# Optimization experiments

Measured on AMD Instinct MI355X. Metric: run time of the kernel, lower is better.

Reference implementation:

```python
import jax, jax.numpy as jnp
import numpy as np

B, N, D, H, O = 8, 2048, 64, 64, 64
ALPHA = 2.0  # LeakyReLU negative slope per module default
NEG = -9e15


def _lin(x, W, b):
    # torch nn.Linear: y = x @ W.T + b, W is [out, in]
    return x @ W.T + b


def setup_inputs() -> dict:
    key = jax.random.key(0)
    ks = jax.random.split(key, 32)
    f32 = jnp.float32
    x = jax.random.normal(ks[0], (B, N, D), f32)
    adj = jax.random.randint(ks[1], (B, N, N), 0, 2).astype(f32)
    c = jax.random.normal(ks[2], (B, N, H), f32)
    h = jax.random.normal(ks[3], (B, N, H), f32)
    s = 0.1
    W = jax.random.normal(ks[4], (D, H), f32) * s           # GAT weight
    a = jax.random.normal(ks[5], (2 * H, 1), f32) * s       # GAT attention vector
    def lin(k, out_d, in_d):
        k1, k2 = jax.random.split(k)
        return (jax.random.normal(k1, (out_d, in_d), f32) * s,
                jax.random.normal(k2, (out_d,), f32) * s)
    Wf, bWf = lin(ks[6], H, H); Wi, bWi = lin(ks[7], H, H)
    Wo, bWo = lin(ks[8], H, H); Wc, bWc = lin(ks[9], H, H)
    Uf, bUf = lin(ks[10], H, D); Ui, bUi = lin(ks[11], H, D)
    Uo, bUo = lin(ks[12], H, D); Uc, bUc = lin(ks[13], H, D)
    Wout, bout = lin(ks[14], O, 2 * H)
    return dict(x=x, adj=adj, c=c, h=h, W=W, a=a,
                Wf=Wf, bWf=bWf, Wi=Wi, bWi=bWi, Wo=Wo, bWo=bWo, Wc=Wc, bWc=bWc,
                Uf=Uf, bUf=bUf, Ui=Ui, bUi=bUi, Uo=Uo, bUo=bUo, Uc=Uc, bUc=bUc,
                Wout=Wout, bout=bout)


def reference(x, adj, c, h, W, a,
              Wf, bWf, Wi, bWi, Wo, bWo, Wc, bWc,
              Uf, bUf, Ui, bUi, Uo, bUo, Uc, bUc,
              Wout, bout):
    # ---- GraphAttentionLayer (eval mode: dropout is identity) ----
    Wh = x @ W                                   # [B,N,H]
    # e[b,i,j] = leakyrelu(a[:H].Wh_i + a[H:].Wh_j) -- same math as the
    a_src = (Wh @ a[:H]).squeeze(-1)             # [B,N]
    a_dst = (Wh @ a[H:]).squeeze(-1)             # [B,N]
    e = jax.nn.leaky_relu(a_src[:, :, None] + a_dst[:, None, :], ALPHA)  # [B,N,N]
    att = jnp.where(adj > 0, e, NEG)
    att = jax.nn.softmax(att, axis=2)
    x_hidden = jax.nn.elu(att @ Wh)              # [B,N,H] (concat=True)
    # ---- LSTMLayer step ----
    f_t = jax.nn.sigmoid(_lin(h, Wf, bWf) + _lin(x, Uf, bUf))
    i_t = jax.nn.sigmoid(_lin(h, Wi, bWi) + _lin(x, Ui, bUi))
    o_t = jax.nn.sigmoid(_lin(h, Wo, bWo) + _lin(x, Uo, bUo))
    c_hat = jnp.tanh(_lin(h, Wc, bWc) + _lin(x, Uc, bUc))
    c_t = f_t * c + i_t * c_hat
    h_t = o_t * jax.nn.relu(c_t)                 # gate = nn.ReLU() default
    total = jnp.concatenate([x_hidden, h_t], axis=2)  # [B,N,2H]
    output = jax.nn.relu(_lin(total, Wout, bout))     # [B,N,O]
    return (output, h_t, c_t)
```

## Files before the change

### kernel.cpp

```cpp
#include <hip/hip_runtime.h>
#include <math.h>

#define B_ 8
#define N_ 2048
#define NT_ (B_*N_)
#define OUTSZ (NT_*64)

#define WS_ASRC  0
#define WS_ADST  (WS_ASRC + NT_)
#define WS_WT    (WS_ADST + NT_)
#define WS_BB    (WS_WT + 128*256)
#define WS_WOT   (WS_BB + 256)
#define WS_PD    (WS_WOT + 128*64)
#define WS_PN    (WS_PD + 8*NT_)

typedef float f32x4 __attribute__((ext_vector_type(4)));
typedef __bf16 bf16x8 __attribute__((ext_vector_type(8)));
typedef __bf16 bf16x4 __attribute__((ext_vector_type(4)));

__device__ __forceinline__ float lrelu2(float x) { return x > 0.f ? x : 2.f * x; }
__device__ __forceinline__ float f4get(const float4& v, int k) { return k==0?v.x:(k==1?v.y:(k==2?v.z:v.w)); }

__global__ __launch_bounds__(256) void k1_wh(const float* __restrict__ x, const float* __restrict__ W,
                                             const float* __restrict__ a, float* __restrict__ ws,
                                             __bf16* __restrict__ whT,
                                             const float* Wf, const float* Wi, const float* Wo, const float* Wc,
                                             const float* Uf, const float* Ui, const float* Uo, const float* Uc,
                                             const float* bWf, const float* bWi, const float* bWo, const float* bWc,
                                             const float* bUf, const float* bUi, const float* bUo, const float* bUc,
                                             const float* Wout)
{
    __shared__ float xl[64 * 68];
    __shared__ float Wl[64 * 68];
    int t = threadIdx.x;
    if (blockIdx.x >= 256) {
        int idx = (blockIdx.x - 256) * 256 + t;
        if (idx < 128 * 256) {
            int k = idx >> 8, o = idx & 255;
            int g = o >> 6, u = o & 63;
            const float* Wg = (g == 0) ? Wf : (g == 1) ? Wi : (g == 2) ? Wo : Wc;
            const float* Ug = (g == 0) ? Uf : (g == 1) ? Ui : (g == 2) ? Uo : Uc;
            ws[WS_WT + idx] = (k < 64) ? Wg[u * 64 + k] : Ug[u * 64 + (k - 64)];
        } else if (idx < 128 * 256 + 256) {
            int o = idx - 128 * 256;
            int g = o >> 6, u = o & 63;
            const float* bW = (g == 0) ? bWf : (g == 1) ? bWi : (g == 2) ? bWo : bWc;
            const float* bU = (g == 0) ? bUf : (g == 1) ? bUi : (g == 2) ? bUo : bUc;
            ws[WS_BB + o] = bW[u] + bU[u];
        } else if (idx < 128 * 256 + 256 + 128 * 64) {
            int j = idx - (128 * 256 + 256);
            int k = j >> 6, u = j & 63;
            ws[WS_WOT + j] = Wout[u * 128 + k];
        }
        return;
    }
    int i0 = blockIdx.x * 64;
    #pragma unroll
    for (int it = 0; it < 4; ++it) {
        int f = t + 256 * it;
        int r = f >> 4, q = f & 15;
        *(float4*)&xl[r * 68 + q * 4] = *(const float4*)&x[i0 * 64 + f * 4];
        *(float4*)&Wl[r * 68 + q * 4] = *(const float4*)&W[f * 4];
    }
    __syncthreads();
    int cg = t & 15, rg = t >> 4;
    int c0 = cg * 4, r0 = rg * 4;
    float acc[4][4] = {};
    #pragma unroll
    for (int d0 = 0; d0 < 64; d0 += 4) {
        float4 wv[4], xv[4];
        #pragma unroll
        for (int k = 0; k < 4; ++k) wv[k] = *(float4*)&Wl[(d0 + k) * 68 + c0];
        #pragma unroll
        for (int ri = 0; ri < 4; ++ri) xv[ri] = *(float4*)&xl[(r0 + ri) * 68 + d0];
        #pragma unroll
        for (int ri = 0; ri < 4; ++ri)
            #pragma unroll
            for (int k = 0; k < 4; ++k) {
                float xs = f4get(xv[ri], k);
                acc[ri][0] += xs * wv[k].x; acc[ri][1] += xs * wv[k].y;
                acc[ri][2] += xs * wv[k].z; acc[ri][3] += xs * wv[k].w;
            }
    }
    int b = i0 >> 11;
    int rowb0 = (i0 & 2047) + r0;
    #pragma unroll
    for (int cj = 0; cj < 4; ++cj) {
        bf16x4 v;
        v[0] = (__bf16)acc[0][cj]; v[1] = (__bf16)acc[1][cj];
        v[2] = (__bf16)acc[2][cj]; v[3] = (__bf16)acc[3][cj];
        *(bf16x4*)&whT[((size_t)(b * 64 + c0 + cj)) * N_ + rowb0] = v;
    }
    float4 a0 = *(const float4*)&a[c0];
    float4 a1 = *(const float4*)&a[64 + c0];
    #pragma unroll
    for (int ri = 0; ri < 4; ++ri) {
        int row = i0 + r0 + ri;
        float s0 = acc[ri][0]*a0.x + acc[ri][1]*a0.y + acc[ri][2]*a0.z + acc[ri][3]*a0.w;
        float s1 = acc[ri][0]*a1.x + acc[ri][1]*a1.y + acc[ri][2]*a1.z + acc[ri][3]*a1.w;
        #pragma unroll
        for (int m = 1; m < 16; m <<= 1) { s0 += __shfl_xor(s0, m, 64); s1 += __shfl_xor(s1, m, 64); }
        if (cg == 0) { ws[WS_ASRC + row] = s0; ws[WS_ADST + row] = s1; }
    }
}

__global__ __launch_bounds__(256) void k2v10(const float* __restrict__ adj,
                                             const __bf16* __restrict__ whT,
                                             float* __restrict__ ws)
{
    __shared__ __bf16 adjt[2][16][268];
    __shared__ float lsa[4][16][68];
    __shared__ float lsd[4][16];
    __shared__ float gred[4];
    int tid = threadIdx.x;
    int lane = tid & 63, w = tid >> 6;
    int r = lane & 15, g = lane >> 4;
    int jr = blockIdx.x & 7;
    int rslab = blockIdx.x >> 3;
    int b = rslab >> 4;
    int row_base = rslab * 128;
    int jbeg = jr * 256 + w * 64;

    {
        float gm = -3.0e38f;
        for (int i = tid; i < N_; i += 256) gm = fmaxf(gm, ws[WS_ADST + b * N_ + i]);
        #pragma unroll
        for (int m_ = 1; m_ < 64; m_ <<= 1) gm = fmaxf(gm, __shfl_xor(gm, m_, 64));
        if (lane == 0) gred[w] = gm;
    }
    __syncthreads();
    float gmax = fmaxf(fmaxf(gred[0], gred[1]), fmaxf(gred[2], gred[3]));

    bf16x8 bfr[2][4];
    #pragma unroll
    for (int ks = 0; ks < 2; ++ks)
        #pragma unroll
        for (int n = 0; n < 4; ++n)
            bfr[ks][n] = *(const bf16x8*)&whT[(size_t)(b * 64 + n * 16 + r) * N_ + jbeg + ks * 32 + g * 8];
    float ejr[2][8];
    #pragma unroll
    for (int ks = 0; ks < 2; ++ks) {
        float4 d0 = *(const float4*)&ws[WS_ADST + b * N_ + jbeg + ks * 32 + g * 8];
        float4 d1 = *(const float4*)&ws[WS_ADST + b * N_ + jbeg + ks * 32 + g * 8 + 4];
        ejr[ks][0]=__expf(d0.x); ejr[ks][1]=__expf(d0.y); ejr[ks][2]=__expf(d0.z); ejr[ks][3]=__expf(d0.w);
        ejr[ks][4]=__expf(d1.x); ejr[ks][5]=__expf(d1.y); ejr[ks][6]=__expf(d1.z); ejr[ks][7]=__expf(d1.w);
    }
    float asv8[8];
    #pragma unroll
    for (int tt = 0; tt < 8; ++tt)
        asv8[tt] = ws[WS_ASRC + row_base + tt * 16 + r];

    f32x4 sreg[2][4];

#define SLOAD(T, S)                                                                        \
    {                                                                                      \
        _Pragma("unroll")                                                                  \
        for (int i = 0; i < 4; ++i)                                                        \
            sreg[S][i] = *(const f32x4*)&adj[(size_t)(row_base + (T) * 16 + w * 4 + i) * N_ \
                                             + jr * 256 + lane * 4];                       \
    }
#define SWRITE(T, S)                                                                       \
    {                                                                                      \
        _Pragma("unroll")                                                                  \
        for (int i = 0; i < 4; ++i) {                                                      \
            bf16x4 bv;                                                                     \
            bv[0] = (__bf16)sreg[S][i][0]; bv[1] = (__bf16)sreg[S][i][1];                  \
            bv[2] = (__bf16)sreg[S][i][2]; bv[3] = (__bf16)sreg[S][i][3];                  \
            *(bf16x4*)&adjt[(T) & 1][w * 4 + i][lane * 4] = bv;                            \
        }                                                                                  \
    }

    SLOAD(0, 0);
    SWRITE(0, 0);
    SLOAD(1, 1);
    asm volatile("s_waitcnt lgkmcnt(0)" ::: "memory");
    __builtin_amdgcn_s_barrier();
    asm volatile("" ::: "memory");

    __bf16* pn = (__bf16*)&ws[WS_PN];

    #pragma unroll
    for (int t = 0; t < 8; ++t) {
        const int s = t & 1;
        if (t + 2 < 8) { SLOAD(t + 2, s); }
        float as = asv8[t];
        float M  = lrelu2(as + gmax);
        float c1 = __expf(as - M);
        float c2 = __expf(2.f * as - M);
        float thr = __expf(-as);
        f32x4 acc[4] = {{0.f,0.f,0.f,0.f},{0.f,0.f,0.f,0.f},{0.f,0.f,0.f,0.f},{0.f,0.f,0.f,0.f}};
        float dsum = 0.f;
        #pragma unroll
        for (int ks = 0; ks < 2; ++ks) {
            bf16x8 at = *(const bf16x8*)&adjt[s][r][w * 64 + ks * 32 + g * 8];
            bf16x8 af;
            float ds_ = 0.f;
            #pragma unroll
            for (int e = 0; e < 8; ++e) {
                float avv = (float)at[e];
                float E = ejr[ks][e];
                float p = (E > thr) ? c1 * E : (c2 * E) * E;
                p = (avv > 0.f) ? p : 0.f;
                ds_ += p;
                af[e] = (__bf16)p;
            }
            dsum += ds_;
            #pragma unroll
            for (int n = 0; n < 4; ++n)
                acc[n] = __builtin_amdgcn_mfma_f32_16x16x32_bf16(af, bfr[ks][n], acc[n], 0, 0, 0);
        }
        dsum += __shfl_xor(dsum, 16, 64);
        dsum += __shfl_xor(dsum, 32, 64);
        #pragma unroll
        for (int n = 0; n < 4; ++n)
            #pragma unroll
            for (int i = 0; i < 4; ++i)
                lsa[w][g * 4 + i][n * 16 + r] = acc[n][i];
        if (g == 0) lsd[w][r] = dsum;
        if (t + 1 < 8) { SWRITE(t + 1, s ^ 1); }
        asm volatile("s_waitcnt lgkmcnt(0)" ::: "memory");
        __builtin_amdgcn_s_barrier();
        asm volatile("" ::: "memory");
        {
            int rl = tid >> 4, h0 = (tid & 15) * 4;
            float4 sv = make_float4(0.f, 0.f, 0.f, 0.f);
            #pragma unroll
            for (int w2 = 0; w2 < 4; ++w2) {
                float4 q = *(const float4*)&lsa[w2][rl][h0];
                sv.x += q.x; sv.y += q.y; sv.z += q.z; sv.w += q.w;
            }
            int row0 = row_base + t * 16;
            bf16x4 bv;
            bv[0] = (__bf16)sv.x; bv[1] = (__bf16)sv.y; bv[2] = (__bf16)sv.z; bv[3] = (__bf16)sv.w;
            *(bf16x4*)&pn[((size_t)jr * NT_ + row0 + rl) * 64 + h0] = bv;
            if (tid < 16)
                ws[WS_PD + jr * NT_ + row0 + tid] =
                    lsd[0][tid] + lsd[1][tid] + lsd[2][tid] + lsd[3][tid];
        }
        asm volatile("s_waitcnt lgkmcnt(0)" ::: "memory");
        __builtin_amdgcn_s_barrier();
        asm volatile("" ::: "memory");
    }
#undef SLOAD
#undef SWRITE
}

__global__ __launch_bounds__(256) void k3_lstm(const float* __restrict__ x, const float* __restrict__ c,
                                               const float* __restrict__ h, const float* __restrict__ ws,
                                               float* __restrict__ out)
{
    __shared__ float Al[16 * 132];
    __shared__ float gl[16 * 260];
    int t = threadIdx.x;
    int base = blockIdx.x * 16;
    {
        int r = t >> 4, k0 = (t & 15) * 8;
        const float* src = (k0 < 64) ? &h[(base + r) * 64 + k0] : &x[(base + r) * 64 + (k0 - 64)];
        *(float4*)&Al[r * 132 + k0]     = *(const float4*)&src[0];
        *(float4*)&Al[r * 132 + k0 + 4] = *(const float4*)&src[4];
    }
    __syncthreads();
    int og = t & 63, rg = t >> 6;
    int o0 = og * 4;
    const float* WT = &ws[WS_WT];
    float acc[4][4] = {};
    #pragma unroll
    for (int k0 = 0; k0 < 128; k0 += 4) {
        float4 wv[4], av[4];
        #pragma unroll
        for (int kk = 0; kk < 4; ++kk) wv[kk] = *(const float4*)&WT[(k0 + kk) * 256 + o0];
        #pragma unroll
        for (int rr = 0; rr < 4; ++rr) av[rr] = *(float4*)&Al[(rg + 4 * rr) * 132 + k0];
        #pragma unroll
        for (int rr = 0; rr < 4; ++rr)
            #pragma unroll
            for (int kk = 0; kk < 4; ++kk) {
                float as = f4get(av[rr], kk);
                acc[rr][0] += as * wv[kk].x; acc[rr][1] += as * wv[kk].y;
                acc[rr][2] += as * wv[kk].z; acc[rr][3] += as * wv[kk].w;
            }
    }
    float4 bbv = *(const float4*)&ws[WS_BB + o0];
    #pragma unroll
    for (int rr = 0; rr < 4; ++rr) {
        int r = rg + 4 * rr;
        *(float4*)&gl[r * 260 + o0] = make_float4(acc[rr][0] + bbv.x, acc[rr][1] + bbv.y,
                                                  acc[rr][2] + bbv.z, acc[rr][3] + bbv.w);
    }
    __syncthreads();
    int u = t & 63, rq = t >> 6;
    #pragma unroll
    for (int pp = 0; pp < 4; ++pp) {
        int r = rq + 4 * pp;
        float gf = gl[r * 260 + u];
        float gi = gl[r * 260 + 64 + u];
        float go = gl[r * 260 + 128 + u];
        float gc = gl[r * 260 + 192 + u];
        float fg = 1.f / (1.f + __expf(-gf));
        float ig = 1.f / (1.f + __expf(-gi));
        float oo = 1.f / (1.f + __expf(-go));
        float ch = tanhf(gc);
        float cv = c[(base + r) * 64 + u];
        float ct = fg * cv + ig * ch;
        float ht = oo * fmaxf(ct, 0.f);
        out[OUTSZ + (base + r) * 64 + u] = ht;
        out[2 * OUTSZ + (base + r) * 64 + u] = ct;
    }
}

__global__ __launch_bounds__(256) void k5b(const float* __restrict__ ws, const float* __restrict__ bout,
                                           float* __restrict__ out)
{
    __shared__ float Al[16 * 132];
    int t = threadIdx.x;
    int base = blockIdx.x * 16;
    const float* ht = &out[OUTSZ];
    const __bf16* pn = (const __bf16*)&ws[WS_PN];
    #pragma unroll
    for (int it = 0; it < 2; ++it) {
        int f = t + 256 * it;
        int r = f >> 5, q = f & 31;
        int k0 = q * 4;
        int row = base + r;
        float4 v;
        if (k0 < 64) {
            float4 s = make_float4(0.f, 0.f, 0.f, 0.f);
            float d = 0.f;
            #pragma unroll
            for (int jr = 0; jr < 8; ++jr) {
                bf16x4 p = *(const bf16x4*)&pn[((size_t)jr * NT_ + row) * 64 + k0];
                s.x += (float)p[0]; s.y += (float)p[1]; s.z += (float)p[2]; s.w += (float)p[3];
                d += ws[WS_PD + jr * NT_ + row];
            }
            float inv = 1.f / d;
            v.x = s.x * inv; v.x = v.x > 0.f ? v.x : expm1f(v.x);
            v.y = s.y * inv; v.y = v.y > 0.f ? v.y : expm1f(v.y);
            v.z = s.z * inv; v.z = v.z > 0.f ? v.z : expm1f(v.z);
            v.w = s.w * inv; v.w = v.w > 0.f ? v.w : expm1f(v.w);
        } else {
            v = *(const float4*)&ht[(size_t)row * 64 + (k0 - 64)];
        }
        *(float4*)&Al[r * 132 + k0] = v;
    }
    __syncthreads();
    int row = t >> 4, cg = t & 15;
    int o0 = cg * 4;
    const float* WT = &ws[WS_WOT];
    float4 acc = make_float4(0.f, 0.f, 0.f, 0.f);
    #pragma unroll 8
    for (int k = 0; k < 128; ++k) {
        float a = Al[row * 132 + k];
        float4 wv = *(const float4*)&WT[k * 64 + o0];
        acc.x += a * wv.x; acc.y += a * wv.y; acc.z += a * wv.z; acc.w += a * wv.w;
    }
    float4 bo = *(const float4*)&bout[o0];
    float4 o;
    o.x = fmaxf(acc.x + bo.x, 0.f);
    o.y = fmaxf(acc.y + bo.y, 0.f);
    o.z = fmaxf(acc.z + bo.z, 0.f);
    o.w = fmaxf(acc.w + bo.w, 0.f);
    *(float4*)&out[(size_t)(base + row) * 64 + o0] = o;
}

extern "C" void kernel_launch(void* const* d_in, const int* in_sizes, int n_in,
                              void* d_out, int out_size, void* d_ws, size_t ws_size,
                              hipStream_t stream)
{
    const float* x    = (const float*)d_in[0];
    const float* adj  = (const float*)d_in[1];
    const float* c    = (const float*)d_in[2];
    const float* h    = (const float*)d_in[3];
    const float* W    = (const float*)d_in[4];
    const float* a    = (const float*)d_in[5];
    const float* Wf   = (const float*)d_in[6];
    const float* bWf  = (const float*)d_in[7];
    const float* Wi   = (const float*)d_in[8];
    const float* bWi  = (const float*)d_in[9];
    const float* Wo   = (const float*)d_in[10];
    const float* bWo  = (const float*)d_in[11];
    const float* Wc   = (const float*)d_in[12];
    const float* bWc  = (const float*)d_in[13];
    const float* Uf   = (const float*)d_in[14];
    const float* bUf  = (const float*)d_in[15];
    const float* Ui   = (const float*)d_in[16];
    const float* bUi  = (const float*)d_in[17];
    const float* Uo   = (const float*)d_in[18];
    const float* bUo  = (const float*)d_in[19];
    const float* Uc   = (const float*)d_in[20];
    const float* bUc  = (const float*)d_in[21];
    const float* Wout = (const float*)d_in[22];
    const float* bout = (const float*)d_in[23];
    float* out = (float*)d_out;
    float* ws  = (float*)d_ws;
    __bf16* whT = (__bf16*)out;

    k1_wh<<<417, 256, 0, stream>>>(x, W, a, ws, whT,
                                   Wf, Wi, Wo, Wc, Uf, Ui, Uo, Uc,
                                   bWf, bWi, bWo, bWc, bUf, bUi, bUo, bUc, Wout);
    k3_lstm<<<NT_ / 16, 256, 0, stream>>>(x, c, h, ws, out);
    k2v10<<<1024, 256, 0, stream>>>(adj, whT, ws);
    k5b<<<NT_ / 16, 256, 0, stream>>>(ws, bout, out);
}
```

Before: 85.84 us.

## Fuse Wh projection and LSTM step into one launch, split weight prep

Weight transposition and bias packing move into a small standalone prep kernel. The GAT Wh projection blocks and the LSTM gate blocks now run as one 1280-block launch that branches on block index and shares one shared-memory buffer. The two independent stages can then overlap on the GPU, which removes the launch gap and tail between them. In exchange, the LSTM blocks reserve the larger shared allocation, which may lower occupancy, and the launch count stays the same.

Result: no change. 86.78 us (+1.1%).

```diff
diff --git a/kernel.cpp b/kernel.cpp
--- a/kernel.cpp
+++ b/kernel.cpp
@@ -21,86 +21,150 @@
 __device__ __forceinline__ float lrelu2(float x) { return x > 0.f ? x : 2.f * x; }
 __device__ __forceinline__ float f4get(const float4& v, int k) { return k==0?v.x:(k==1?v.y:(k==2?v.z:v.w)); }
 
-__global__ __launch_bounds__(256) void k1_wh(const float* __restrict__ x, const float* __restrict__ W,
-                                             const float* __restrict__ a, float* __restrict__ ws,
-                                             __bf16* __restrict__ whT,
-                                             const float* Wf, const float* Wi, const float* Wo, const float* Wc,
-                                             const float* Uf, const float* Ui, const float* Uo, const float* Uc,
-                                             const float* bWf, const float* bWi, const float* bWo, const float* bWc,
-                                             const float* bUf, const float* bUi, const float* bUo, const float* bUc,
-                                             const float* Wout)
+__global__ void k0_prep(const float* Wf, const float* Wi, const float* Wo, const float* Wc,
+                        const float* Uf, const float* Ui, const float* Uo, const float* Uc,
+                        const float* bWf, const float* bWi, const float* bWo, const float* bWc,
+                        const float* bUf, const float* bUi, const float* bUo, const float* bUc,
+                        const float* Wout, float* ws)
 {
-    __shared__ float xl[64 * 68];
-    __shared__ float Wl[64 * 68];
+    int idx = blockIdx.x * 256 + threadIdx.x;
+    if (idx < 128 * 256) {
+        int k = idx >> 8, o = idx & 255;
+        int g = o >> 6, u = o & 63;
+        const float* Wg = (g == 0) ? Wf : (g == 1) ? Wi : (g == 2) ? Wo : Wc;
+        const float* Ug = (g == 0) ? Uf : (g == 1) ? Ui : (g == 2) ? Uo : Uc;
+        ws[WS_WT + idx] = (k < 64) ? Wg[u * 64 + k] : Ug[u * 64 + (k - 64)];
+    } else if (idx < 128 * 256 + 256) {
+        int o = idx - 128 * 256;
+        int g = o >> 6, u = o & 63;
+        const float* bW = (g == 0) ? bWf : (g == 1) ? bWi : (g == 2) ? bWo : bWc;
+        const float* bU = (g == 0) ? bUf : (g == 1) ? bUi : (g == 2) ? bUo : bUc;
+        ws[WS_BB + o] = bW[u] + bU[u];
+    } else if (idx < 128 * 256 + 256 + 128 * 64) {
+        int j = idx - (128 * 256 + 256);
+        int k = j >> 6, u = j & 63;
+        ws[WS_WOT + j] = Wout[u * 128 + k];
+    }
+}
+
+__global__ __launch_bounds__(256) void k13(const float* __restrict__ x, const float* __restrict__ W,
+                                           const float* __restrict__ a, float* __restrict__ ws,
+                                           __bf16* __restrict__ whT,
+                                           const float* __restrict__ c, const float* __restrict__ h,
+                                           float* __restrict__ out)
+{
+    __shared__ float smem[2 * 64 * 68];
     int t = threadIdx.x;
-    if (blockIdx.x >= 256) {
-        int idx = (blockIdx.x - 256) * 256 + t;
-        if (idx < 128 * 256) {
-            int k = idx >> 8, o = idx & 255;
-            int g = o >> 6, u = o & 63;
-            const float* Wg = (g == 0) ? Wf : (g == 1) ? Wi : (g == 2) ? Wo : Wc;
-            const float* Ug = (g == 0) ? Uf : (g == 1) ? Ui : (g == 2) ? Uo : Uc;
-            ws[WS_WT + idx] = (k < 64) ? Wg[u * 64 + k] : Ug[u * 64 + (k - 64)];
-        } else if (idx < 128 * 256 + 256) {
-            int o = idx - 128 * 256;
-            int g = o >> 6, u = o & 63;
-            const float* bW = (g == 0) ? bWf : (g == 1) ? bWi : (g == 2) ? bWo : bWc;
-            const float* bU = (g == 0) ? bUf : (g == 1) ? bUi : (g == 2) ? bUo : bUc;
-            ws[WS_BB + o] = bW[u] + bU[u];
-        } else if (idx < 128 * 256 + 256 + 128 * 64) {
-            int j = idx - (128 * 256 + 256);
-            int k = j >> 6, u = j & 63;
-            ws[WS_WOT + j] = Wout[u * 128 + k];
+
+    if (blockIdx.x < 256) {
+        float* xl = smem;
+        float* Wl = smem + 64 * 68;
+        int i0 = blockIdx.x * 64;
+        #pragma unroll
+        for (int it = 0; it < 4; ++it) {
+            int f = t + 256 * it;
+            int r = f >> 4, q = f & 15;
+            *(float4*)&xl[r * 68 + q * 4] = *(const float4*)&x[i0 * 64 + f * 4];
+            *(float4*)&Wl[r * 68 + q * 4] = *(const float4*)&W[f * 4];
+        }
+        __syncthreads();
+        int cg = t & 15, rg = t >> 4;
+        int c0 = cg * 4, r0 = rg * 4;
+        float acc[4][4] = {};
+        #pragma unroll
+        for (int d0 = 0; d0 < 64; d0 += 4) {
+            float4 wv[4], xv[4];
+            #pragma unroll
+            for (int k = 0; k < 4; ++k) wv[k] = *(float4*)&Wl[(d0 + k) * 68 + c0];
+            #pragma unroll
+            for (int ri = 0; ri < 4; ++ri) xv[ri] = *(float4*)&xl[(r0 + ri) * 68 + d0];
+            #pragma unroll
+            for (int ri = 0; ri < 4; ++ri)
+                #pragma unroll
+                for (int k = 0; k < 4; ++k) {
+                    float xs = f4get(xv[ri], k);
+                    acc[ri][0] += xs * wv[k].x; acc[ri][1] += xs * wv[k].y;
+                    acc[ri][2] += xs * wv[k].z; acc[ri][3] += xs * wv[k].w;
+                }
+        }
+        int b = i0 >> 11;
+        int rowb0 = (i0 & 2047) + r0;
+        #pragma unroll
+        for (int cj = 0; cj < 4; ++cj) {
+            bf16x4 v;
+            v[0] = (__bf16)acc[0][cj]; v[1] = (__bf16)acc[1][cj];
+            v[2] = (__bf16)acc[2][cj]; v[3] = (__bf16)acc[3][cj];
+            *(bf16x4*)&whT[((size_t)(b * 64 + c0 + cj)) * N_ + rowb0] = v;
+        }
+        float4 a0 = *(const float4*)&a[c0];
+        float4 a1 = *(const float4*)&a[64 + c0];
+        #pragma unroll
+        for (int ri = 0; ri < 4; ++ri) {
+            int row = i0 + r0 + ri;
+            float s0 = acc[ri][0]*a0.x + acc[ri][1]*a0.y + acc[ri][2]*a0.z + acc[ri][3]*a0.w;
+            float s1 = acc[ri][0]*a1.x + acc[ri][1]*a1.y + acc[ri][2]*a1.z + acc[ri][3]*a1.w;
+            #pragma unroll
+            for (int m = 1; m < 16; m <<= 1) { s0 += __shfl_xor(s0, m, 64); s1 += __shfl_xor(s1, m, 64); }
+            if (cg == 0) { ws[WS_ASRC + row] = s0; ws[WS_ADST + row] = s1; }
         }
         return;
     }
-    int i0 = blockIdx.x * 64;
-    #pragma unroll
-    for (int it = 0; it < 4; ++it) {
-        int f = t + 256 * it;
-        int r = f >> 4, q = f & 15;
-        *(float4*)&xl[r * 68 + q * 4] = *(const float4*)&x[i0 * 64 + f * 4];
-        *(float4*)&Wl[r * 68 + q * 4] = *(const float4*)&W[f * 4];
+
+    float* Al = smem;
+    float* gl = smem + 16 * 132;
+    int base = (blockIdx.x - 256) * 16;
+    {
+        int r = t >> 4, k0 = (t & 15) * 8;
+        const float* src = (k0 < 64) ? &h[(base + r) * 64 + k0] : &x[(base + r) * 64 + (k0 - 64)];
+        *(float4*)&Al[r * 132 + k0]     = *(const float4*)&src[0];
+        *(float4*)&Al[r * 132 + k0 + 4] = *(const float4*)&src[4];
     }
     __syncthreads();
-    int cg = t & 15, rg = t >> 4;
-    int c0 = cg * 4, r0 = rg * 4;
+    int og = t & 63, rg = t >> 6;
+    int o0 = og * 4;
+    const float* WT = &ws[WS_WT];
     float acc[4][4] = {};
     #pragma unroll
-    for (int d0 = 0; d0 < 64; d0 += 4) {
-        float4 wv[4], xv[4];
-        #pragma unroll
-        for (int k = 0; k < 4; ++k) wv[k] = *(float4*)&Wl[(d0 + k) * 68 + c0];
-        #pragma unroll
-        for (int ri = 0; ri < 4; ++ri) xv[ri] = *(float4*)&xl[(r0 + ri) * 68 + d0];
-        #pragma unroll
-        for (int ri = 0; ri < 4; ++ri)
-            #pragma unroll
-            for (int k = 0; k < 4; ++k) {
-                float xs = f4get(xv[ri], k);
-                acc[ri][0] += xs * wv[k].x; acc[ri][1] += xs * wv[k].y;
-                acc[ri][2] += xs * wv[k].z; acc[ri][3] += xs * wv[k].w;
+    for (int k0 = 0; k0 < 128; k0 += 4) {
+        float4 wv[4], av[4];
+        #pragma unroll
+        for (int kk = 0; kk < 4; ++kk) wv[kk] = *(const float4*)&WT[(k0 + kk) * 256 + o0];
+        #pragma unroll
+        for (int rr = 0; rr < 4; ++rr) av[rr] = *(float4*)&Al[(rg + 4 * rr) * 132 + k0];
+        #pragma unroll
+        for (int rr = 0; rr < 4; ++rr)
+            #pragma unroll
+            for (int kk = 0; kk < 4; ++kk) {
+                float as = f4get(av[rr], kk);
+                acc[rr][0] += as * wv[kk].x; acc[rr][1] += as * wv[kk].y;
+                acc[rr][2] += as * wv[kk].z; acc[rr][3] += as * wv[kk].w;
             }
     }
-    int b = i0 >> 11;
-    int rowb0 = (i0 & 2047) + r0;
-    #pragma unroll
-    for (int cj = 0; cj < 4; ++cj) {
-        bf16x4 v;
-        v[0] = (__bf16)acc[0][cj]; v[1] = (__bf16)acc[1][cj];
-        v[2] = (__bf16)acc[2][cj]; v[3] = (__bf16)acc[3][cj];
-        *(bf16x4*)&whT[((size_t)(b * 64 + c0 + cj)) * N_ + rowb0] = v;
-    }
-    float4 a0 = *(const float4*)&a[c0];
-    float4 a1 = *(const float4*)&a[64 + c0];
-    #pragma unroll
-    for (int ri = 0; ri < 4; ++ri) {
-        int row = i0 + r0 + ri;
-        float s0 = acc[ri][0]*a0.x + acc[ri][1]*a0.y + acc[ri][2]*a0.z + acc[ri][3]*a0.w;
-        float s1 = acc[ri][0]*a1.x + acc[ri][1]*a1.y + acc[ri][2]*a1.z + acc[ri][3]*a1.w;
-        #pragma unroll
-        for (int m = 1; m < 16; m <<= 1) { s0 += __shfl_xor(s0, m, 64); s1 += __shfl_xor(s1, m, 64); }
-        if (cg == 0) { ws[WS_ASRC + row] = s0; ws[WS_ADST + row] = s1; }
+    float4 bbv = *(const float4*)&ws[WS_BB + o0];
+    #pragma unroll
+    for (int rr = 0; rr < 4; ++rr) {
+        int r = rg + 4 * rr;
+        *(float4*)&gl[r * 260 + o0] = make_float4(acc[rr][0] + bbv.x, acc[rr][1] + bbv.y,
+                                                  acc[rr][2] + bbv.z, acc[rr][3] + bbv.w);
+    }
+    __syncthreads();
+    int u = t & 63, rq = t >> 6;
+    #pragma unroll
+    for (int pp = 0; pp < 4; ++pp) {
+        int r = rq + 4 * pp;
+        float gf = gl[r * 260 + u];
+        float gi = gl[r * 260 + 64 + u];
+        float go = gl[r * 260 + 128 + u];
+        float gc = gl[r * 260 + 192 + u];
+        float fg = 1.f / (1.f + __expf(-gf));
+        float ig = 1.f / (1.f + __expf(-gi));
+        float oo = 1.f / (1.f + __expf(-go));
+        float ch = tanhf(gc);
+        float cv = c[(base + r) * 64 + u];
+        float ct = fg * cv + ig * ch;
+        float ht = oo * fmaxf(ct, 0.f);
+        out[OUTSZ + (base + r) * 64 + u] = ht;
+        out[2 * OUTSZ + (base + r) * 64 + u] = ct;
     }
 }
 
@@ -243,69 +307,6 @@
     }
 #undef SLOAD
 #undef SWRITE
-}
-
-__global__ __launch_bounds__(256) void k3_lstm(const float* __restrict__ x, const float* __restrict__ c,
-                                               const float* __restrict__ h, const float* __restrict__ ws,
-                                               float* __restrict__ out)
-{
-    __shared__ float Al[16 * 132];
-    __shared__ float gl[16 * 260];
-    int t = threadIdx.x;
-    int base = blockIdx.x * 16;
-    {
-        int r = t >> 4, k0 = (t & 15) * 8;
-        const float* src = (k0 < 64) ? &h[(base + r) * 64 + k0] : &x[(base + r) * 64 + (k0 - 64)];
-        *(float4*)&Al[r * 132 + k0]     = *(const float4*)&src[0];
-        *(float4*)&Al[r * 132 + k0 + 4] = *(const float4*)&src[4];
-    }
-    __syncthreads();
-    int og = t & 63, rg = t >> 6;
-    int o0 = og * 4;
-    const float* WT = &ws[WS_WT];
-    float acc[4][4] = {};
-    #pragma unroll
-    for (int k0 = 0; k0 < 128; k0 += 4) {
-        float4 wv[4], av[4];
-        #pragma unroll
-        for (int kk = 0; kk < 4; ++kk) wv[kk] = *(const float4*)&WT[(k0 + kk) * 256 + o0];
-        #pragma unroll
-        for (int rr = 0; rr < 4; ++rr) av[rr] = *(float4*)&Al[(rg + 4 * rr) * 132 + k0];
-        #pragma unroll
-        for (int rr = 0; rr < 4; ++rr)
-            #pragma unroll
-            for (int kk = 0; kk < 4; ++kk) {
-                float as = f4get(av[rr], kk);
-                acc[rr][0] += as * wv[kk].x; acc[rr][1] += as * wv[kk].y;
-                acc[rr][2] += as * wv[kk].z; acc[rr][3] += as * wv[kk].w;
-            }
-    }
-    float4 bbv = *(const float4*)&ws[WS_BB + o0];
-    #pragma unroll
-    for (int rr = 0; rr < 4; ++rr) {
-        int r = rg + 4 * rr;
-        *(float4*)&gl[r * 260 + o0] = make_float4(acc[rr][0] + bbv.x, acc[rr][1] + bbv.y,
-                                                  acc[rr][2] + bbv.z, acc[rr][3] + bbv.w);
-    }
-    __syncthreads();
-    int u = t & 63, rq = t >> 6;
-    #pragma unroll
-    for (int pp = 0; pp < 4; ++pp) {
-        int r = rq + 4 * pp;
-        float gf = gl[r * 260 + u];
-        float gi = gl[r * 260 + 64 + u];
-        float go = gl[r * 260 + 128 + u];
-        float gc = gl[r * 260 + 192 + u];
-        float fg = 1.f / (1.f + __expf(-gf));
-        float ig = 1.f / (1.f + __expf(-gi));
-        float oo = 1.f / (1.f + __expf(-go));
-        float ch = tanhf(gc);
-        float cv = c[(base + r) * 64 + u];
-        float ct = fg * cv + ig * ch;
-        float ht = oo * fmaxf(ct, 0.f);
-        out[OUTSZ + (base + r) * 64 + u] = ht;
-        out[2 * OUTSZ + (base + r) * 64 + u] = ct;
-    }
 }
 
 __global__ __launch_bounds__(256) void k5b(const float* __restrict__ ws, const float* __restrict__ bout,
@@ -394,10 +395,9 @@
     float* ws  = (float*)d_ws;
     __bf16* whT = (__bf16*)out;
 
-    k1_wh<<<417, 256, 0, stream>>>(x, W, a, ws, whT,
-                                   Wf, Wi, Wo, Wc, Uf, Ui, Uo, Uc,
-                                   bWf, bWi, bWo, bWc, bUf, bUi, bUo, bUc, Wout);
-    k3_lstm<<<NT_ / 16, 256, 0, stream>>>(x, c, h, ws, out);
+    k0_prep<<<161, 256, 0, stream>>>(Wf, Wi, Wo, Wc, Uf, Ui, Uo, Uc,
+                                     bWf, bWi, bWo, bWc, bUf, bUi, bUo, bUc, Wout, ws);
+    k13<<<1280, 256, 0, stream>>>(x, W, a, ws, whT, c, h, out);
     k2v10<<<1024, 256, 0, stream>>>(adj, whT, ws);
     k5b<<<NT_ / 16, 256, 0, stream>>>(ws, bout, out);
 }
```
